# Performance work log

Hardware: AMD Instinct MI355X
Metric: run time of the kernel (lower is better)

The kernel has to match this reference:

```python
import jax, jax.numpy as jnp
import numpy as np

N_NODES = 100000

def setup_inputs() -> dict:
    key = jax.random.key(0)
    k1, k2, k3 = jax.random.split(key, 3)
    x = jax.random.normal(k1, (N_NODES, 128), dtype=jnp.float32)
    edge_index = jax.random.randint(k2, (2, 1600000), 0, N_NODES, dtype=jnp.int64)
    W = jax.random.normal(k3, (128, 128), dtype=jnp.float32) * 0.05  # Linear weight [out, in]
    b = jnp.zeros((128,), dtype=jnp.float32)
    return {"x": x, "edge_index": edge_index, "W": W, "b": b}

def reference(x, edge_index, W, b):
    # GCNConv (PyG defaults): normalize=True, add_self_loops=True, bias=True.
    N = x.shape[0]
    # 1) linear transform (no bias inside)
    h = x @ W.T  # [N, H]
    # 2) add self loops
    loops = jnp.arange(N, dtype=edge_index.dtype)
    src = jnp.concatenate([edge_index[0], loops])  # source (x_j)
    dst = jnp.concatenate([edge_index[1], loops])  # target (aggregation)
    # 3) symmetric degree normalization: deg over target nodes with unit weights
    deg = jax.ops.segment_sum(jnp.ones_like(dst, dtype=h.dtype), dst, num_segments=N)
    dinv = jnp.where(deg > 0, jax.lax.rsqrt(deg), 0.0)
    norm = dinv[src] * dinv[dst]  # [E+N]
    # 4) gather-scale-scatter aggregation
    msgs = h[src] * norm[:, None]  # [E+N, H]
    out = jax.ops.segment_sum(msgs, dst, num_segments=N)
    # 5) bias
    return out + b
```

## Files before the change

### kernel.cpp

```cpp
#include <hip/hip_runtime.h>

#define H 128
#define NREG 8
#define KE 16
#define TILE (256 * KE)
#define B2T 2048
#define SCAP 3072
#define RCAP 220160

typedef __attribute__((ext_vector_type(8))) short short8_t;
typedef __attribute__((ext_vector_type(4))) float float4_t;

__device__ __forceinline__ ushort f2bf(float f) {
  uint u = __float_as_uint(f);
  u += 0x7fff + ((u >> 16) & 1);
  return (ushort)(u >> 16);
}
__device__ __forceinline__ float bflo(uint v) { return __uint_as_float(v << 16); }
__device__ __forceinline__ float bfhi(uint v) { return __uint_as_float(v & 0xffff0000u); }

__global__ __launch_bounds__(256) void k_bin(const int* __restrict__ src, const int* __restrict__ dst,
                                             int* gcur, int* __restrict__ breg, int E, int npr) {
  __shared__ int cntw[4][NREG];
  __shared__ int basew[4][NREG];
  __shared__ int lpre8[NREG + 1];
  __shared__ int gbase8[NREG];
  __shared__ int staged[TILE];
  const int tid = threadIdx.x;
  const int wv = tid >> 6;
  if (tid < 32) cntw[tid >> 3][tid & 7] = 0;
  __syncthreads();
  const int base = blockIdx.x * TILE;
  int pk[KE], r[KE], off[KE];
  #pragma unroll
  for (int k = 0; k < KE; ++k) {
    const int e = base + k * 256 + tid;
    if (e < E) {
      const int s = src[e], d = dst[e];
      r[k] = (int)((unsigned)d / (unsigned)npr);
      pk[k] = (s << 14) | (d - r[k] * npr);
      off[k] = atomicAdd(&cntw[wv][r[k]], 1);
    } else r[k] = -1;
  }
  __syncthreads();
  if (tid == 0) {
    int acc = 0;
    #pragma unroll
    for (int j = 0; j < NREG; ++j) {
      lpre8[j] = acc;
      #pragma unroll
      for (int w2 = 0; w2 < 4; ++w2) { basew[w2][j] = acc; acc += cntw[w2][j]; }
    }
    lpre8[NREG] = acc;
  }
  __syncthreads();
  if (tid < NREG) gbase8[tid] = atomicAdd(&gcur[tid], lpre8[tid + 1] - lpre8[tid]);
  #pragma unroll
  for (int k = 0; k < KE; ++k)
    if (r[k] >= 0) staged[basew[wv][r[k]] + off[k]] = pk[k];
  __syncthreads();
  const int tot = lpre8[NREG];
  for (int i = tid; i < tot; i += 256) {
    int reg = 0;
    #pragma unroll
    for (int j = 1; j < NREG; ++j) reg += (i >= lpre8[j]);
    const int p = gbase8[reg] + (i - lpre8[reg]);
    if (p < RCAP) breg[reg * RCAP + p] = staged[i];
  }
}

__global__ __launch_bounds__(256) void k_bin2(const int* __restrict__ breg, const int* __restrict__ gcur,
                                              int* cur2, int* __restrict__ bsub, int nsub) {
  __shared__ int cnt[128], lcur[128], lpre[128], gb[128];
  __shared__ int staged[B2T];
  const int tid = threadIdx.x;
  const int r = blockIdx.x & 7;
  const int t0 = (blockIdx.x >> 3) * B2T;
  const int total = min(gcur[r], RCAP);
  if (t0 >= total) return;
  const int cntT = min(B2T, total - t0);
  for (int i = tid; i < 128; i += 256) { cnt[i] = 0; lcur[i] = 0; }
  __syncthreads();
  const int* bp = breg + (size_t)r * RCAP + t0;
  for (int i = tid; i < cntT; i += 256) atomicAdd(&cnt[(bp[i] >> 7) & 127], 1);
  __syncthreads();
  if (tid < 128) lpre[tid] = cnt[tid];
  __syncthreads();
  for (int off = 1; off < 128; off <<= 1) {
    int v = 0;
    if (tid < 128 && tid >= off) v = lpre[tid - off];
    __syncthreads();
    if (tid < 128) lpre[tid] += v;
    __syncthreads();
  }
  if (tid < 128) {
    lpre[tid] -= cnt[tid];
    const int c = cnt[tid];
    gb[tid] = c ? atomicAdd(&cur2[r * nsub + tid], c) : 0;
  }
  __syncthreads();
  for (int i = tid; i < cntT; i += 256) {
    const int v = bp[i];
    const int sub = (v >> 7) & 127;
    const int pos = lpre[sub] + atomicAdd(&lcur[sub], 1);
    staged[pos] = (sub << 24) | ((v >> 14) << 7) | (v & 127);
  }
  __syncthreads();
  for (int i = tid; i < cntT; i += 256) {
    const int v = staged[i];
    const int sub = (int)((unsigned)v >> 24);
    const int pos = gb[sub] + (i - lpre[sub]);
    if (pos < SCAP) bsub[((size_t)(r * nsub + sub)) * SCAP + pos] = v & 0xFFFFFF;
  }
}

__global__ __launch_bounds__(256) void k_fill3(const int* __restrict__ bsub, const int* __restrict__ cur2,
                                               float* __restrict__ dinv, uint4* __restrict__ rowinfo,
                                               int* __restrict__ csr, int N, int npr, int nsub) {
  __shared__ int cnt[128], pre[128], lcur[128];
  __shared__ int stage[SCAP], sorted[SCAP];
  const int tid = threadIdx.x;
  const int r = blockIdx.x & 7;
  const int sub = blockIdx.x >> 3;
  const int sid = r * nsub + sub;
  const int gn0 = r * npr + sub * 128;
  int nodes = npr - sub * 128; if (nodes > 128) nodes = 128;
  if (N - gn0 < nodes) nodes = N - gn0;
  if (nodes <= 0) return;
  if (tid < 128) cnt[tid] = 0;
  __syncthreads();

  const int slotbase = sid * SCAP;
  const int cc = min(cur2[sid], SCAP);
  const int* bp = bsub + (size_t)slotbase;
  for (int i = tid; i < cc; i += 256) {
    const int v = bp[i];
    stage[i] = v;
    atomicAdd(&cnt[v & 127], 1);
  }
  __syncthreads();

  if (tid < 128) pre[tid] = cnt[tid];
  __syncthreads();
  for (int off = 1; off < 128; off <<= 1) {
    int v = 0;
    if (tid < 128 && tid >= off) v = pre[tid - off];
    __syncthreads();
    if (tid < 128) pre[tid] += v;
    __syncthreads();
  }
  if (tid < 128) pre[tid] -= cnt[tid];
  __syncthreads();

  if (tid < nodes) {
    const int c = cnt[tid];
    const float dv = rsqrtf((float)(1 + c));
    dinv[gn0 + tid] = dv;
    rowinfo[gn0 + tid] = make_uint4((uint)(slotbase + pre[tid]), (uint)c, __float_as_uint(dv), 0u);
    lcur[tid] = pre[tid];
  }
  __syncthreads();

  for (int i = tid; i < cc; i += 256) {
    const int v = stage[i];
    const int p = atomicAdd(&lcur[v & 127], 1);
    sorted[p] = (int)((unsigned)v >> 7);
  }
  __syncthreads();
  for (int i = tid; i < cc; i += 256) csr[slotbase + i] = sorted[i];
}

__global__ __launch_bounds__(256) void k_linear(const float* __restrict__ x, const float* __restrict__ W,
                                                const float* __restrict__ dinv, ushort* __restrict__ hs, int N) {
  const int tid  = threadIdx.x;
  const int lane = tid & 63;
  const int wid  = tid >> 6;
  const int rg   = wid >> 1;
  const int cg   = wid & 1;
  const int q    = lane >> 4;
  const int lm   = lane & 15;

  short8_t bfr[4][4];
  #pragma unroll
  for (int kk = 0; kk < 4; ++kk) {
    #pragma unroll
    for (int nf = 0; nf < 4; ++nf) {
      const float* wp = W + (cg * 64 + nf * 16 + lm) * 128 + kk * 32 + q * 8;
      float4_t w0 = *(const float4_t*)wp;
      float4_t w1 = *(const float4_t*)(wp + 4);
      union { short8_t s; ushort u[8]; } t;
      t.u[0] = f2bf(w0.x); t.u[1] = f2bf(w0.y); t.u[2] = f2bf(w0.z); t.u[3] = f2bf(w0.w);
      t.u[4] = f2bf(w1.x); t.u[5] = f2bf(w1.y); t.u[6] = f2bf(w1.z); t.u[7] = f2bf(w1.w);
      bfr[kk][nf] = t.s;
    }
  }

  const int ntiles = (N + 31) / 32;
  for (int tile = blockIdx.x; tile < ntiles; tile += gridDim.x) {
    const int n0 = tile * 32;
    const int arow = n0 + rg * 16 + lm;
    const int arow_c = (arow < N) ? arow : (N - 1);
    const float* xp = x + (long)arow_c * H + q * 8;
    short8_t afr[4];
    #pragma unroll
    for (int kk = 0; kk < 4; ++kk) {
      float4_t x0 = *(const float4_t*)(xp + kk * 32);
      float4_t x1 = *(const float4_t*)(xp + kk * 32 + 4);
      union { short8_t s; ushort u[8]; } t;
      t.u[0] = f2bf(x0.x); t.u[1] = f2bf(x0.y); t.u[2] = f2bf(x0.z); t.u[3] = f2bf(x0.w);
      t.u[4] = f2bf(x1.x); t.u[5] = f2bf(x1.y); t.u[6] = f2bf(x1.z); t.u[7] = f2bf(x1.w);
      afr[kk] = t.s;
    }

    float4_t acc[4];
    #pragma unroll
    for (int nf = 0; nf < 4; ++nf) acc[nf] = (float4_t){0.f, 0.f, 0.f, 0.f};
    #pragma unroll
    for (int kk = 0; kk < 4; ++kk) {
      #pragma unroll
      for (int nf = 0; nf < 4; ++nf)
        acc[nf] = __builtin_amdgcn_mfma_f32_16x16x32_bf16(bfr[kk][nf], afr[kk], acc[nf], 0, 0, 0);
    }

    if (arow < N) {
      const float dv = dinv[arow];
      ushort* hrow = hs + (size_t)arow * H + cg * 64 + q * 4;
      #pragma unroll
      for (int nf = 0; nf < 4; ++nf) {
        uint pk = (uint)f2bf(acc[nf][0] * dv) | ((uint)f2bf(acc[nf][1] * dv) << 16);
        uint pk2 = (uint)f2bf(acc[nf][2] * dv) | ((uint)f2bf(acc[nf][3] * dv) << 16);
        uint2 o; o.x = pk; o.y = pk2;
        *(uint2*)(hrow + nf * 16) = o;
      }
    }
  }
}

#define ACC8(q) { a0 += bflo((q).x); a1 += bfhi((q).x); a2 += bflo((q).y); a3 += bfhi((q).y); \
                  a4 += bflo((q).z); a5 += bfhi((q).z); a6 += bflo((q).w); a7 += bfhi((q).w); }
__global__ __launch_bounds__(256) void k_agg(const ushort* __restrict__ hs,
                                             const uint4* __restrict__ rowinfo, const int* __restrict__ csr,
                                             const float* __restrict__ bias, float* __restrict__ out,
                                             int N, int npr) {
  const int r = blockIdx.x & 7;
  const int ln = (blockIdx.x >> 3) * 16 + (threadIdx.x >> 4);
  if (ln >= npr) return;
  const int d = r * npr + ln;
  if (d >= N) return;
  const int j = threadIdx.x & 15;
  const uint4* hp = (const uint4*)hs;

  const uint4 info = rowinfo[d];
  int i = (int)info.x;
  int cnt = (int)info.y;
  const float dd = __uint_as_float(info.z);

  const uint4 qs = hp[(size_t)d * 16 + j];
  float a0 = bflo(qs.x), a1 = bfhi(qs.x), a2 = bflo(qs.y), a3 = bfhi(qs.y);
  float a4 = bflo(qs.z), a5 = bfhi(qs.z), a6 = bflo(qs.w), a7 = bfhi(qs.w);

  for (; cnt >= 8; cnt -= 8, i += 8) {
    const int s0 = csr[i],     s1 = csr[i + 1], s2 = csr[i + 2], s3 = csr[i + 3];
    const int s4 = csr[i + 4], s5 = csr[i + 5], s6 = csr[i + 6], s7 = csr[i + 7];
    const uint4 qA = hp[(size_t)s0 * 16 + j];
    const uint4 qB = hp[(size_t)s1 * 16 + j];
    const uint4 qC = hp[(size_t)s2 * 16 + j];
    const uint4 qD = hp[(size_t)s3 * 16 + j];
    const uint4 qE = hp[(size_t)s4 * 16 + j];
    const uint4 qF = hp[(size_t)s5 * 16 + j];
    const uint4 qG = hp[(size_t)s6 * 16 + j];
    const uint4 qH = hp[(size_t)s7 * 16 + j];
    ACC8(qA) ACC8(qB) ACC8(qC) ACC8(qD) ACC8(qE) ACC8(qF) ACC8(qG) ACC8(qH)
  }
  if (cnt >= 4) {
    const int s0 = csr[i], s1 = csr[i + 1], s2 = csr[i + 2], s3 = csr[i + 3];
    const uint4 qA = hp[(size_t)s0 * 16 + j];
    const uint4 qB = hp[(size_t)s1 * 16 + j];
    const uint4 qC = hp[(size_t)s2 * 16 + j];
    const uint4 qD = hp[(size_t)s3 * 16 + j];
    ACC8(qA) ACC8(qB) ACC8(qC) ACC8(qD)
    cnt -= 4; i += 4;
  }
  for (; cnt > 0; --cnt, ++i) {
    const uint4 q = hp[(size_t)csr[i] * 16 + j];
    ACC8(q)
  }

  const float4_t b0 = *(const float4_t*)(bias + j * 8);
  const float4_t b1 = *(const float4_t*)(bias + j * 8 + 4);
  float4_t o0, o1;
  o0.x = a0 * dd + b0.x; o0.y = a1 * dd + b0.y; o0.z = a2 * dd + b0.z; o0.w = a3 * dd + b0.w;
  o1.x = a4 * dd + b1.x; o1.y = a5 * dd + b1.y; o1.z = a6 * dd + b1.z; o1.w = a7 * dd + b1.w;
  __builtin_nontemporal_store(o0, (float4_t*)(out + (size_t)d * H + j * 8));
  __builtin_nontemporal_store(o1, (float4_t*)(out + (size_t)d * H + j * 8 + 4));
}

extern "C" void kernel_launch(void* const* d_in, const int* in_sizes, int n_in,
                              void* d_out, int out_size, void* d_ws, size_t ws_size,
                              hipStream_t stream) {
  const float* x = (const float*)d_in[0];
  const int*   edge = (const int*)d_in[1];
  const float* W = (const float*)d_in[2];
  const float* b = (const float*)d_in[3];
  float* out = (float*)d_out;

  const int N = in_sizes[0] / H;
  const int E = in_sizes[1] / 2;
  const int* src = edge;
  const int* dst = edge + E;
  const int npr  = (N + NREG - 1) / NREG;
  const int nsub = (npr + 127) / 128;
  const int nsubt = NREG * nsub;

  char* w = (char*)d_ws;
  ushort* hs     = (ushort*)w;  w += (size_t)N * H * 2;
  float*  dinv   = (float*)w;   w += (size_t)N * 4;
  int*    gcur   = (int*)w;     w += (size_t)NREG * 4;
  int*    cur2   = (int*)w;     w += (size_t)nsubt * 4;
  uint4*  rowinfo= (uint4*)w;   w += (size_t)N * 16;
  int*    csr    = (int*)w;     w += (size_t)nsubt * SCAP * 4;
  int*    breg   = (int*)w;     w += (size_t)NREG * RCAP * 4;
  int*    bsub   = (int*)w;     w += (size_t)nsubt * SCAP * 4;
  (void)ws_size;

  (void)hipMemsetAsync(gcur, 0, (size_t)(NREG + nsubt) * 4, stream);

  const int nbin = (E + TILE - 1) / TILE;
  const int bpr2 = (RCAP + B2T - 1) / B2T;
  k_bin<<<nbin, 256, 0, stream>>>(src, dst, gcur, breg, E, npr);
  k_bin2<<<8 * bpr2, 256, 0, stream>>>(breg, gcur, cur2, bsub, nsub);
  k_fill3<<<nsubt, 256, 0, stream>>>(bsub, cur2, dinv, rowinfo, csr, N, npr, nsub);
  k_linear<<<512, 256, 0, stream>>>(x, W, dinv, hs, N);
  k_agg<<<8 * ((npr + 15) / 16), 256, 0, stream>>>(hs, rowinfo, csr, b, out, N, npr);
}
```

Before: 134.5 us.

## Fuse linear transform into binning kernel and move source dinv scaling into aggregation

The linear transform no longer depends on the degree computation. It now runs as the first 512 blocks of the binning kernel, so the GEMM overlaps with edge binning and one launch is dropped. Because of this, the per-source dinv scaling moves out of the linear epilogue and into the aggregation loop, which does an extra gathered dinv load and an FMA per edge. The trade is GEMM/binning concurrency against the extra random loads in the gather-heavy aggregation, and the bf16 values of h are no longer pre-scaled.

```diff
diff --git a/kernel.cpp b/kernel.cpp
--- a/kernel.cpp
+++ b/kernel.cpp
@@ -4,6 +4,7 @@
 #define NREG 8
 #define KE 16
 #define TILE (256 * KE)
+#define LINB 512
 #define B2T 2048
 #define SCAP 3072
 #define RCAP 220160
@@ -19,53 +20,121 @@
 __device__ __forceinline__ float bflo(uint v) { return __uint_as_float(v << 16); }
 __device__ __forceinline__ float bfhi(uint v) { return __uint_as_float(v & 0xffff0000u); }
 
-__global__ __launch_bounds__(256) void k_bin(const int* __restrict__ src, const int* __restrict__ dst,
-                                             int* gcur, int* __restrict__ breg, int E, int npr) {
+__global__ __launch_bounds__(256) void k_linbin(const float* __restrict__ x, const float* __restrict__ W,
+                                                ushort* __restrict__ hs,
+                                                const int* __restrict__ src, const int* __restrict__ dst,
+                                                int* gcur, int* __restrict__ breg,
+                                                int N, int E, int npr) {
   __shared__ int cntw[4][NREG];
   __shared__ int basew[4][NREG];
   __shared__ int lpre8[NREG + 1];
   __shared__ int gbase8[NREG];
   __shared__ int staged[TILE];
   const int tid = threadIdx.x;
-  const int wv = tid >> 6;
-  if (tid < 32) cntw[tid >> 3][tid & 7] = 0;
-  __syncthreads();
-  const int base = blockIdx.x * TILE;
-  int pk[KE], r[KE], off[KE];
-  #pragma unroll
-  for (int k = 0; k < KE; ++k) {
-    const int e = base + k * 256 + tid;
-    if (e < E) {
-      const int s = src[e], d = dst[e];
-      r[k] = (int)((unsigned)d / (unsigned)npr);
-      pk[k] = (s << 14) | (d - r[k] * npr);
-      off[k] = atomicAdd(&cntw[wv][r[k]], 1);
-    } else r[k] = -1;
-  }
-  __syncthreads();
-  if (tid == 0) {
-    int acc = 0;
+
+  if (blockIdx.x < LINB) {
+    const int lane = tid & 63;
+    const int wid  = tid >> 6;
+    const int rg   = wid >> 1;
+    const int cg   = wid & 1;
+    const int q    = lane >> 4;
+    const int lm   = lane & 15;
+
+    short8_t bfr[4][4];
     #pragma unroll
-    for (int j = 0; j < NREG; ++j) {
-      lpre8[j] = acc;
-      #pragma unroll
-      for (int w2 = 0; w2 < 4; ++w2) { basew[w2][j] = acc; acc += cntw[w2][j]; }
-    }
-    lpre8[NREG] = acc;
-  }
-  __syncthreads();
-  if (tid < NREG) gbase8[tid] = atomicAdd(&gcur[tid], lpre8[tid + 1] - lpre8[tid]);
-  #pragma unroll
-  for (int k = 0; k < KE; ++k)
-    if (r[k] >= 0) staged[basew[wv][r[k]] + off[k]] = pk[k];
-  __syncthreads();
-  const int tot = lpre8[NREG];
-  for (int i = tid; i < tot; i += 256) {
-    int reg = 0;
+    for (int kk = 0; kk < 4; ++kk) {
+      #pragma unroll
+      for (int nf = 0; nf < 4; ++nf) {
+        const float* wp = W + (cg * 64 + nf * 16 + lm) * 128 + kk * 32 + q * 8;
+        float4_t w0 = *(const float4_t*)wp;
+        float4_t w1 = *(const float4_t*)(wp + 4);
+        union { short8_t s; ushort u[8]; } t;
+        t.u[0] = f2bf(w0.x); t.u[1] = f2bf(w0.y); t.u[2] = f2bf(w0.z); t.u[3] = f2bf(w0.w);
+        t.u[4] = f2bf(w1.x); t.u[5] = f2bf(w1.y); t.u[6] = f2bf(w1.z); t.u[7] = f2bf(w1.w);
+        bfr[kk][nf] = t.s;
+      }
+    }
+
+    const int ntiles = (N + 31) / 32;
+    for (int tile = blockIdx.x; tile < ntiles; tile += LINB) {
+      const int n0 = tile * 32;
+      const int arow = n0 + rg * 16 + lm;
+      const int arow_c = (arow < N) ? arow : (N - 1);
+      const float* xp = x + (long)arow_c * H + q * 8;
+      short8_t afr[4];
+      #pragma unroll
+      for (int kk = 0; kk < 4; ++kk) {
+        float4_t x0 = *(const float4_t*)(xp + kk * 32);
+        float4_t x1 = *(const float4_t*)(xp + kk * 32 + 4);
+        union { short8_t s; ushort u[8]; } t;
+        t.u[0] = f2bf(x0.x); t.u[1] = f2bf(x0.y); t.u[2] = f2bf(x0.z); t.u[3] = f2bf(x0.w);
+        t.u[4] = f2bf(x1.x); t.u[5] = f2bf(x1.y); t.u[6] = f2bf(x1.z); t.u[7] = f2bf(x1.w);
+        afr[kk] = t.s;
+      }
+
+      float4_t acc[4];
+      #pragma unroll
+      for (int nf = 0; nf < 4; ++nf) acc[nf] = (float4_t){0.f, 0.f, 0.f, 0.f};
+      #pragma unroll
+      for (int kk = 0; kk < 4; ++kk) {
+        #pragma unroll
+        for (int nf = 0; nf < 4; ++nf)
+          acc[nf] = __builtin_amdgcn_mfma_f32_16x16x32_bf16(bfr[kk][nf], afr[kk], acc[nf], 0, 0, 0);
+      }
+
+      if (arow < N) {
+        ushort* hrow = hs + (size_t)arow * H + cg * 64 + q * 4;
+        #pragma unroll
+        for (int nf = 0; nf < 4; ++nf) {
+          uint2 o;
+          o.x = (uint)f2bf(acc[nf][0]) | ((uint)f2bf(acc[nf][1]) << 16);
+          o.y = (uint)f2bf(acc[nf][2]) | ((uint)f2bf(acc[nf][3]) << 16);
+          *(uint2*)(hrow + nf * 16) = o;
+        }
+      }
+    }
+  } else {
+    const int bb = blockIdx.x - LINB;
+    const int wv = tid >> 6;
+    if (tid < 32) cntw[tid >> 3][tid & 7] = 0;
+    __syncthreads();
+    const int base = bb * TILE;
+    int pk[KE], r[KE], off[KE];
     #pragma unroll
-    for (int j = 1; j < NREG; ++j) reg += (i >= lpre8[j]);
-    const int p = gbase8[reg] + (i - lpre8[reg]);
-    if (p < RCAP) breg[reg * RCAP + p] = staged[i];
+    for (int k = 0; k < KE; ++k) {
+      const int e = base + k * 256 + tid;
+      if (e < E) {
+        const int s = src[e], d = dst[e];
+        r[k] = (int)((unsigned)d / (unsigned)npr);
+        pk[k] = (s << 14) | (d - r[k] * npr);
+        off[k] = atomicAdd(&cntw[wv][r[k]], 1);
+      } else r[k] = -1;
+    }
+    __syncthreads();
+    if (tid == 0) {
+      int acc = 0;
+      #pragma unroll
+      for (int j = 0; j < NREG; ++j) {
+        lpre8[j] = acc;
+        #pragma unroll
+        for (int w2 = 0; w2 < 4; ++w2) { basew[w2][j] = acc; acc += cntw[w2][j]; }
+      }
+      lpre8[NREG] = acc;
+    }
+    __syncthreads();
+    if (tid < NREG) gbase8[tid] = atomicAdd(&gcur[tid], lpre8[tid + 1] - lpre8[tid]);
+    #pragma unroll
+    for (int k = 0; k < KE; ++k)
+      if (r[k] >= 0) staged[basew[wv][r[k]] + off[k]] = pk[k];
+    __syncthreads();
+    const int tot = lpre8[NREG];
+    for (int i = tid; i < tot; i += 256) {
+      int reg = 0;
+      #pragma unroll
+      for (int j = 1; j < NREG; ++j) reg += (i >= lpre8[j]);
+      const int p = gbase8[reg] + (i - lpre8[reg]);
+      if (p < RCAP) breg[reg * RCAP + p] = staged[i];
+    }
   }
 }
 
@@ -170,75 +239,11 @@
   for (int i = tid; i < cc; i += 256) csr[slotbase + i] = sorted[i];
 }
 
-__global__ __launch_bounds__(256) void k_linear(const float* __restrict__ x, const float* __restrict__ W,
-                                                const float* __restrict__ dinv, ushort* __restrict__ hs, int N) {
-  const int tid  = threadIdx.x;
-  const int lane = tid & 63;
-  const int wid  = tid >> 6;
-  const int rg   = wid >> 1;
-  const int cg   = wid & 1;
-  const int q    = lane >> 4;
-  const int lm   = lane & 15;
-
-  short8_t bfr[4][4];
-  #pragma unroll
-  for (int kk = 0; kk < 4; ++kk) {
-    #pragma unroll
-    for (int nf = 0; nf < 4; ++nf) {
-      const float* wp = W + (cg * 64 + nf * 16 + lm) * 128 + kk * 32 + q * 8;
-      float4_t w0 = *(const float4_t*)wp;
-      float4_t w1 = *(const float4_t*)(wp + 4);
-      union { short8_t s; ushort u[8]; } t;
-      t.u[0] = f2bf(w0.x); t.u[1] = f2bf(w0.y); t.u[2] = f2bf(w0.z); t.u[3] = f2bf(w0.w);
-      t.u[4] = f2bf(w1.x); t.u[5] = f2bf(w1.y); t.u[6] = f2bf(w1.z); t.u[7] = f2bf(w1.w);
-      bfr[kk][nf] = t.s;
-    }
-  }
-
-  const int ntiles = (N + 31) / 32;
-  for (int tile = blockIdx.x; tile < ntiles; tile += gridDim.x) {
-    const int n0 = tile * 32;
-    const int arow = n0 + rg * 16 + lm;
-    const int arow_c = (arow < N) ? arow : (N - 1);
-    const float* xp = x + (long)arow_c * H + q * 8;
-    short8_t afr[4];
-    #pragma unroll
-    for (int kk = 0; kk < 4; ++kk) {
-      float4_t x0 = *(const float4_t*)(xp + kk * 32);
-      float4_t x1 = *(const float4_t*)(xp + kk * 32 + 4);
-      union { short8_t s; ushort u[8]; } t;
-      t.u[0] = f2bf(x0.x); t.u[1] = f2bf(x0.y); t.u[2] = f2bf(x0.z); t.u[3] = f2bf(x0.w);
-      t.u[4] = f2bf(x1.x); t.u[5] = f2bf(x1.y); t.u[6] = f2bf(x1.z); t.u[7] = f2bf(x1.w);
-      afr[kk] = t.s;
-    }
-
-    float4_t acc[4];
-    #pragma unroll
-    for (int nf = 0; nf < 4; ++nf) acc[nf] = (float4_t){0.f, 0.f, 0.f, 0.f};
-    #pragma unroll
-    for (int kk = 0; kk < 4; ++kk) {
-      #pragma unroll
-      for (int nf = 0; nf < 4; ++nf)
-        acc[nf] = __builtin_amdgcn_mfma_f32_16x16x32_bf16(bfr[kk][nf], afr[kk], acc[nf], 0, 0, 0);
-    }
-
-    if (arow < N) {
-      const float dv = dinv[arow];
-      ushort* hrow = hs + (size_t)arow * H + cg * 64 + q * 4;
-      #pragma unroll
-      for (int nf = 0; nf < 4; ++nf) {
-        uint pk = (uint)f2bf(acc[nf][0] * dv) | ((uint)f2bf(acc[nf][1] * dv) << 16);
-        uint pk2 = (uint)f2bf(acc[nf][2] * dv) | ((uint)f2bf(acc[nf][3] * dv) << 16);
-        uint2 o; o.x = pk; o.y = pk2;
-        *(uint2*)(hrow + nf * 16) = o;
-      }
-    }
-  }
-}
-
-#define ACC8(q) { a0 += bflo((q).x); a1 += bfhi((q).x); a2 += bflo((q).y); a3 += bfhi((q).y); \
-                  a4 += bflo((q).z); a5 += bfhi((q).z); a6 += bflo((q).w); a7 += bfhi((q).w); }
-__global__ __launch_bounds__(256) void k_agg(const ushort* __restrict__ hs,
+#define ACCS(q, ds) { a0 = fmaf(bflo((q).x), ds, a0); a1 = fmaf(bfhi((q).x), ds, a1); \
+                      a2 = fmaf(bflo((q).y), ds, a2); a3 = fmaf(bfhi((q).y), ds, a3); \
+                      a4 = fmaf(bflo((q).z), ds, a4); a5 = fmaf(bfhi((q).z), ds, a5); \
+                      a6 = fmaf(bflo((q).w), ds, a6); a7 = fmaf(bfhi((q).w), ds, a7); }
+__global__ __launch_bounds__(256) void k_agg(const ushort* __restrict__ hs, const float* __restrict__ dinv,
                                              const uint4* __restrict__ rowinfo, const int* __restrict__ csr,
                                              const float* __restrict__ bias, float* __restrict__ out,
                                              int N, int npr) {
@@ -256,12 +261,14 @@
   const float dd = __uint_as_float(info.z);
 
   const uint4 qs = hp[(size_t)d * 16 + j];
-  float a0 = bflo(qs.x), a1 = bfhi(qs.x), a2 = bflo(qs.y), a3 = bfhi(qs.y);
-  float a4 = bflo(qs.z), a5 = bfhi(qs.z), a6 = bflo(qs.w), a7 = bfhi(qs.w);
+  float a0 = bflo(qs.x) * dd, a1 = bfhi(qs.x) * dd, a2 = bflo(qs.y) * dd, a3 = bfhi(qs.y) * dd;
+  float a4 = bflo(qs.z) * dd, a5 = bfhi(qs.z) * dd, a6 = bflo(qs.w) * dd, a7 = bfhi(qs.w) * dd;
 
   for (; cnt >= 8; cnt -= 8, i += 8) {
     const int s0 = csr[i],     s1 = csr[i + 1], s2 = csr[i + 2], s3 = csr[i + 3];
     const int s4 = csr[i + 4], s5 = csr[i + 5], s6 = csr[i + 6], s7 = csr[i + 7];
+    const float d0 = dinv[s0], d1 = dinv[s1], d2 = dinv[s2], d3 = dinv[s3];
+    const float d4 = dinv[s4], d5 = dinv[s5], d6 = dinv[s6], d7 = dinv[s7];
     const uint4 qA = hp[(size_t)s0 * 16 + j];
     const uint4 qB = hp[(size_t)s1 * 16 + j];
     const uint4 qC = hp[(size_t)s2 * 16 + j];
@@ -270,20 +277,24 @@
     const uint4 qF = hp[(size_t)s5 * 16 + j];
     const uint4 qG = hp[(size_t)s6 * 16 + j];
     const uint4 qH = hp[(size_t)s7 * 16 + j];
-    ACC8(qA) ACC8(qB) ACC8(qC) ACC8(qD) ACC8(qE) ACC8(qF) ACC8(qG) ACC8(qH)
+    ACCS(qA, d0) ACCS(qB, d1) ACCS(qC, d2) ACCS(qD, d3)
+    ACCS(qE, d4) ACCS(qF, d5) ACCS(qG, d6) ACCS(qH, d7)
   }
   if (cnt >= 4) {
     const int s0 = csr[i], s1 = csr[i + 1], s2 = csr[i + 2], s3 = csr[i + 3];
+    const float d0 = dinv[s0], d1 = dinv[s1], d2 = dinv[s2], d3 = dinv[s3];
     const uint4 qA = hp[(size_t)s0 * 16 + j];
     const uint4 qB = hp[(size_t)s1 * 16 + j];
     const uint4 qC = hp[(size_t)s2 * 16 + j];
     const uint4 qD = hp[(size_t)s3 * 16 + j];
-    ACC8(qA) ACC8(qB) ACC8(qC) ACC8(qD)
+    ACCS(qA, d0) ACCS(qB, d1) ACCS(qC, d2) ACCS(qD, d3)
     cnt -= 4; i += 4;
   }
   for (; cnt > 0; --cnt, ++i) {
-    const uint4 q = hp[(size_t)csr[i] * 16 + j];
-    ACC8(q)
+    const int s = csr[i];
+    const float ds = dinv[s];
+    const uint4 q = hp[(size_t)s * 16 + j];
+    ACCS(q, ds)
   }
 
   const float4_t b0 = *(const float4_t*)(bias + j * 8);
@@ -327,9 +338,8 @@
 
   const int nbin = (E + TILE - 1) / TILE;
   const int bpr2 = (RCAP + B2T - 1) / B2T;
-  k_bin<<<nbin, 256, 0, stream>>>(src, dst, gcur, breg, E, npr);
+  k_linbin<<<LINB + nbin, 256, 0, stream>>>(x, W, hs, src, dst, gcur, breg, N, E, npr);
   k_bin2<<<8 * bpr2, 256, 0, stream>>>(breg, gcur, cur2, bsub, nsub);
   k_fill3<<<nsubt, 256, 0, stream>>>(bsub, cur2, dinv, rowinfo, csr, N, npr, nsub);
-  k_linear<<<512, 256, 0, stream>>>(x, W, dinv, hs, N);
-  k_agg<<<8 * ((npr + 15) / 16), 256, 0, stream>>>(hs, rowinfo, csr, b, out, N, npr);
-}
+  k_agg<<<8 * ((npr + 15) / 16), 256, 0, stream>>>(hs, dinv, rowinfo, csr, b, out, N, npr);
+}
```

Result: faster. 127.3 us (-5.4%).
